# Kernel optimization log

Measured on AMD Instinct MI355X. Metric: run time of the kernel, lower is better.

The kernel has to match this reference:

```python
import jax, jax.numpy as jnp
import numpy as np

N = 50000      # num nodes
C_IN = 128     # channels[0]
C_OUT = 128    # channels[1]
D = 16         # fixed node degree
T = 4          # diffusion steps
H_MLP = 64     # diff_mlp hidden
H_GRU = 128    # GRUAggr hidden
EPS = 0.01


def setup_inputs() -> dict:
    key = jax.random.key(0)
    ks = jax.random.split(key, 10)
    node_attr = jax.random.normal(ks[0], (N, C_IN), jnp.float32)
    # adjacency sorted by source: node i owns columns [i*D, i*D+D)
    src = jnp.repeat(jnp.arange(N), D)
    dst = jax.random.randint(ks[1], (N * D,), 0, N)
    edge_index = jnp.stack([src, dst])                       # [2, N*D]
    slices = jnp.stack([jnp.arange(N) * D, jnp.full((N,), D)], axis=1)  # [N,2] (start,count)
    noise = EPS * jax.random.normal(ks[2], (T, N, D), jnp.float32)      # eps*randn per step
    init = lambda k, shape, fan: (jax.random.normal(k, shape, jnp.float32) / np.sqrt(fan))
    W1 = init(ks[3], ((1 + T) * C_IN, H_MLP), (1 + T) * C_IN)
    b1 = jnp.zeros((H_MLP,), jnp.float32)
    W2 = init(ks[4], (H_MLP, 1), H_MLP)
    b2 = jnp.zeros((1,), jnp.float32)
    Wx = init(ks[5], (C_IN, 3 * H_GRU), C_IN)
    Wh = init(ks[6], (H_GRU, 3 * H_GRU), H_GRU)
    bx = jnp.zeros((3 * H_GRU,), jnp.float32)
    bh = jnp.zeros((3 * H_GRU,), jnp.float32)
    Wo = init(ks[7], (H_GRU, C_OUT), H_GRU)
    bo = jnp.zeros((C_OUT,), jnp.float32)
    return dict(node_attr=node_attr, edge_index=edge_index, slices=slices, noise=noise,
                W1=W1, b1=b1, W2=W2, b2=b2, Wx=Wx, Wh=Wh, bx=bx, bh=bh, Wo=Wo, bo=bo)


def _gru(x_seq, Wx, Wh, bx, bh):
    # x_seq: [T+1, N, C]; torch GRU gate order (r, z, n)
    H = Wh.shape[0]
    def step(h, x):
        gx = x @ Wx + bx
        gh = h @ Wh + bh
        xr, xz, xn = jnp.split(gx, 3, axis=-1)
        hr, hz, hn = jnp.split(gh, 3, axis=-1)
        r = jax.nn.sigmoid(xr + hr)
        z = jax.nn.sigmoid(xz + hz)
        n = jnp.tanh(xn + r * hn)
        return (1.0 - z) * n + z * h, None
    h0 = jnp.zeros((x_seq.shape[1], H), x_seq.dtype)
    h, _ = jax.lax.scan(step, h0, x_seq)
    return h


def reference(node_attr, edge_index, slices, noise, W1, b1, W2, b2, Wx, Wh, bx, bh, Wo, bo):
    n, C = node_attr.shape
    t_steps, _, deg = noise.shape
    dst = edge_index[1]
    walk_embeds = jnp.zeros((n, 1 + t_steps, C), node_attr.dtype).at[:, 0, :].set(node_attr)
    cur = jnp.arange(n)
    for t in range(t_steps):
        starts = slices[cur, 0]                              # slice_cat(adj, adj_slic_t)
        nbr = dst[starts[:, None] + jnp.arange(deg)]         # [N, D] neighbor node ids
        v_t = node_attr[nbr]                                 # [N, D, C]
        # diff_mlp on [prefix walk embed | candidate neighbor]: split the first
        # linear layer so the shared prefix is computed once per node (position
        # 1+t of walk_embeds is still zero, matching the original fill order).
        h_pre = walk_embeds.reshape(n, (1 + t_steps) * C) @ W1 + b1       # [N, H_MLP]
        h_nbr = jnp.einsum('ndc,ch->ndh', v_t, W1[(1 + t) * C:(2 + t) * C])
        logp = (jax.nn.relu(h_pre[:, None, :] + h_nbr) @ W2)[..., 0] + b2[0]  # [N, D]
        logp = jax.lax.stop_gradient(logp)                   # torch.no_grad()
        # scatter_logsumexp over init node == logsumexp over the D candidates
        p = jnp.exp(logp - jax.nn.logsumexp(logp, axis=1, keepdims=True)) + noise[t]
        sel = jnp.argmax(p, axis=1)                          # scatter_max per init node
        cur = nbr[jnp.arange(n), sel]                        # walks_t
        walk_embeds = walk_embeds.at[:, 1 + t, :].set(node_attr[cur])
    h = _gru(jnp.transpose(walk_embeds, (1, 0, 2)), Wx, Wh, bx, bh)
    return h @ Wo + bo                                       # [N, C_OUT]
```

## Files before the change

### kernel.cpp

```cpp
#include <hip/hip_runtime.h>
#include <math.h>

#define NND 50000
#define DEG 16

typedef __attribute__((ext_vector_type(8))) short short8v;
typedef __attribute__((ext_vector_type(4))) float float4v;

#define OFF_HPRE 0ULL
#define OFF_PROJ 12800000ULL
#define OFF_XB   64000000ULL
#define OFF_IDX  102400000ULL
#define OFF_BQF  103600384ULL
#define OFF_WOF  103862528ULL
#define WS_NEED  103895296ULL

#define LOG2E 1.44269504088896f

__device__ __forceinline__ float fast_sig(float x){
    return __builtin_amdgcn_rcpf(1.f + __builtin_amdgcn_exp2f(-LOG2E*x));
}
__device__ __forceinline__ float fast_tanh(float x){
    return fmaf(-2.f, __builtin_amdgcn_rcpf(1.f + __builtin_amdgcn_exp2f((2.f*LOG2E)*x)), 1.f);
}
__device__ __forceinline__ unsigned short f2bf(float f){
    unsigned int u = __float_as_uint(f);
    u += 0x7FFFu + ((u >> 16) & 1u);
    return (unsigned short)(u >> 16);
}
__device__ __forceinline__ float bf2f(unsigned short h){
    return __uint_as_float(((unsigned int)h) << 16);
}

__global__ __launch_bounds__(256) void k_iota(int* __restrict__ idx0){
    int i = blockIdx.x*256 + threadIdx.x;
    if (i < NND) idx0[i] = i;
}

__global__ __launch_bounds__(256) void k_projall(const float* __restrict__ A,
    const float* __restrict__ W1, const float* __restrict__ b1,
    float* __restrict__ hpre, float* __restrict__ proj)
{
    __shared__ float Alt[32][320];
    __shared__ float Bl[32][68];
    const int tid = threadIdx.x;
    const int row0 = blockIdx.x << 8;
    const int y = blockIdx.y;
    const float* B = W1 + (size_t)y*128*64;
    const int row_t = tid >> 4, col_t = tid & 15;
    float4 acc[16];
#pragma unroll
    for (int i=0;i<16;i++) acc[i] = make_float4(0.f,0.f,0.f,0.f);

    for (int k0 = 0; k0 < 128; k0 += 32){
        {
            int gr = row0 + tid; if (gr >= NND) gr = NND-1;
            const float* ap = A + (size_t)gr*128 + k0;
            const int sr = tid + ((tid>>4)<<2);
#pragma unroll
            for (int u=0;u<8;u++){
                float4 v = *(const float4*)(ap + (u<<2));
                Alt[(u<<2)+0][sr] = v.x; Alt[(u<<2)+1][sr] = v.y;
                Alt[(u<<2)+2][sr] = v.z; Alt[(u<<2)+3][sr] = v.w;
            }
        }
#pragma unroll
        for (int r=0;r<2;r++){
            int p = (r<<8) + tid;
            int bk = p >> 4, bc = (p & 15) << 2;
            *(float4*)(&Bl[bk][bc]) = *(const float4*)(B + (size_t)(k0+bk)*64 + bc);
        }
        __syncthreads();
#pragma unroll 2
        for (int k=0;k<32;k++){
            const float* ar = &Alt[k][row_t*20];
            float4 a0 = *(const float4*)(ar);
            float4 a1 = *(const float4*)(ar+4);
            float4 a2 = *(const float4*)(ar+8);
            float4 a3 = *(const float4*)(ar+12);
            float4 b  = *(const float4*)(&Bl[k][col_t<<2]);
            float aa[16] = {a0.x,a0.y,a0.z,a0.w, a1.x,a1.y,a1.z,a1.w,
                            a2.x,a2.y,a2.z,a2.w, a3.x,a3.y,a3.z,a3.w};
#pragma unroll
            for (int j=0;j<16;j++){
                acc[j].x = fmaf(aa[j], b.x, acc[j].x);
                acc[j].y = fmaf(aa[j], b.y, acc[j].y);
                acc[j].z = fmaf(aa[j], b.z, acc[j].z);
                acc[j].w = fmaf(aa[j], b.w, acc[j].w);
            }
        }
        __syncthreads();
    }
    float4 bb = make_float4(0.f,0.f,0.f,0.f);
    if (y == 0) bb = *(const float4*)(b1 + (col_t<<2));
    float* dstp = (y == 0) ? hpre : (proj + (size_t)(y-1)*NND*64);
#pragma unroll
    for (int j=0;j<16;j++){
        int gr = row0 + (row_t<<4) + j;
        if (gr < NND){
            float4 o = make_float4(acc[j].x+bb.x, acc[j].y+bb.y, acc[j].z+bb.z, acc[j].w+bb.w);
            *(float4*)(dstp + ((size_t)gr<<6) + (col_t<<2)) = o;
        }
    }
}

__global__ __launch_bounds__(256) void k_walk4(
    const float* __restrict__ hpre0, const float* __restrict__ proj,
    const int* __restrict__ dst, const float* __restrict__ W2,
    const float* __restrict__ b2, const float* __restrict__ noise,
    int* __restrict__ idxb)
{
    const int tid = threadIdx.x;
    const int sg = tid >> 4, l = tid & 15;
    const int gi = (blockIdx.x << 4) + sg;
    float4 hp = *(const float4*)(hpre0 + ((size_t)gi<<6) + (l<<2));
    float4 w2 = *(const float4*)(W2 + (l<<2));
    const float b2s = b2[0];
    int curv = gi;
#pragma unroll 1
    for (int t=0; t<4; t++){
        const float* pj = proj + (size_t)t*NND*64;
        const int nbr = dst[curv*DEG + l];
        float4 val[16];
#pragma unroll
        for (int d=0; d<16; d++){
            int nd = __shfl(nbr, d, 16);
            val[d] = *(const float4*)(pj + ((size_t)nd<<6) + (l<<2));
        }
        float lp = 0.f;
#pragma unroll
        for (int d=0; d<16; d++){
            float4 v = val[d];
            float q =  fmaxf(hp.x+v.x,0.f)*w2.x;
            q = fmaf(fmaxf(hp.y+v.y,0.f), w2.y, q);
            q = fmaf(fmaxf(hp.z+v.z,0.f), w2.z, q);
            q = fmaf(fmaxf(hp.w+v.w,0.f), w2.w, q);
            q += __shfl_xor(q, 1, 16);
            q += __shfl_xor(q, 2, 16);
            q += __shfl_xor(q, 4, 16);
            q += __shfl_xor(q, 8, 16);
            if (l == d) lp = q + b2s;
        }
        float mx = lp;
#pragma unroll
        for (int off=8; off; off>>=1) mx = fmaxf(mx, __shfl_xor(mx, off, 16));
        float s = expf(lp - mx);
#pragma unroll
        for (int off=8; off; off>>=1) s += __shfl_xor(s, off, 16);
        float p = expf(lp - mx - logf(s)) + noise[(size_t)t*NND*DEG + ((size_t)gi<<4) + l];
        float bv = p; int bi = l;
#pragma unroll
        for (int off=8; off; off>>=1){
            float ov = __shfl_xor(bv, off, 16);
            int   oi = __shfl_xor(bi, off, 16);
            if (ov > bv || (ov == bv && oi < bi)){ bv = ov; bi = oi; }
        }
        int sel = __shfl(nbr, bi, 16);
        if (l == 0) idxb[(size_t)(t+1)*NND + gi] = sel;
        float4 u = *(const float4*)(pj + ((size_t)sel<<6) + (l<<2));
        hp.x += u.x; hp.y += u.y; hp.z += u.z; hp.w += u.w;
        curv = sel;
    }
}

__global__ __launch_bounds__(256) void k_pack_x(const float* __restrict__ na,
    unsigned short* __restrict__ Xb)
{
    int i = blockIdx.x*256 + threadIdx.x;
    if (i < NND*32){
        float4 v = *(const float4*)(na + (size_t)i*4);
        unsigned long long pk = (unsigned long long)f2bf(v.x)
            | ((unsigned long long)f2bf(v.y) << 16)
            | ((unsigned long long)f2bf(v.z) << 32)
            | ((unsigned long long)f2bf(v.w) << 48);
        *(unsigned long long*)(Xb + (size_t)i*4) = pk;
    }
}

__global__ __launch_bounds__(256) void k_pack_bqf(const float* __restrict__ Wx,
    const float* __restrict__ Wh, unsigned short* __restrict__ BqF)
{
    int i = blockIdx.x*256 + threadIdx.x;
    int jj = i & 7, lane = (i>>3)&63, ct = (i>>9)&7, c = (i>>12)&7, y = i>>15;
    int g = ct>>1, jh = ct&1, mm = lane&15, quad = lane>>4;
    int jg = (y<<5) + (jh<<4) + mm;
    int k = (c<<5) + (quad<<3) + jj;
    float v = 0.f;
    if (k < 128){
        if (g < 3) v = Wh[k*384 + g*128 + jg];
    } else {
        int kk = k - 128;
        if (g == 0)      v = Wx[kk*384 + jg];
        else if (g == 1) v = Wx[kk*384 + 128 + jg];
        else if (g == 3) v = Wx[kk*384 + 256 + jg];
    }
    BqF[i] = f2bf(v);
}

__global__ __launch_bounds__(256) void k_pack_wof(const float* __restrict__ Wo,
    unsigned short* __restrict__ WoF)
{
    int i = blockIdx.x*256 + threadIdx.x;
    int jj = i & 7, lane = (i>>3)&63, ct = (i>>9)&7, c = i>>12;
    int n = (ct<<4) + (lane&15);
    int k = (c<<5) + ((lane>>4)<<3) + jj;
    WoF[i] = f2bf(Wo[k*128 + n]);
}

__global__ __launch_bounds__(256,2) void k_gru5(
    const unsigned short* __restrict__ Xb,
    const unsigned short* __restrict__ BqF,
    const unsigned short* __restrict__ WoF,
    const float* __restrict__ bx, const float* __restrict__ bh,
    const float* __restrict__ bo, const int* __restrict__ idxb,
    float* __restrict__ out)
{
    __shared__ unsigned short A_l[8192];
    __shared__ unsigned short X_l[16384];
    const int tid = threadIdx.x;
    const int w = tid >> 6, lane = tid & 63;
    const int m = lane & 15, quad = lane >> 4;
    const int row0 = blockIdx.x << 6;
    const int r = tid & 63, q = tid >> 6;
    int gr = row0 + r; if (gr >= NND) gr = NND-1;
    const int rt_s = r >> 4, m_s = r & 15;
    float brr[2], bzz[2], bxn[2], bhn[2];
#pragma unroll
    for (int jh=0; jh<2; jh++){
        int j = (w<<5) + (jh<<4) + m;
        brr[jh] = bx[j] + bh[j];
        bzz[jh] = bx[128+j] + bh[128+j];
        bxn[jh] = bx[256+j];
        bhn[jh] = bh[256+j];
    }
    unsigned short holdv[2][4][4];
    short8v xv[4];
    {
        const int xr = idxb[gr];
        const unsigned short* xrow = Xb + (size_t)xr*128 + (q<<5);
#pragma unroll
        for (int u=0;u<4;u++) xv[u] = *(const short8v*)(xrow + (u<<3));
#pragma unroll
        for (int u=0;u<4;u++)
            *(short8v*)(X_l + (((rt_s<<2)+q)*64 + (u<<4) + m_s)*8) = xv[u];
        const int xr1 = idxb[NND + gr];
        const unsigned short* xrow1 = Xb + (size_t)xr1*128 + (q<<5);
#pragma unroll
        for (int u=0;u<4;u++) xv[u] = *(const short8v*)(xrow1 + (u<<3));
    }
    __syncthreads();

#pragma unroll 1
    for (int s=0; s<5; s++){
        const unsigned short* Xcur = X_l + ((s&1)<<13);
        float4v zero = {0.f,0.f,0.f,0.f};
        float4v acc[32];
#pragma unroll
        for (int i=0;i<32;i++) acc[i] = zero;
        if (s > 0){
#pragma unroll 1
            for (int c=0;c<4;c++){
                short8v afr[4];
#pragma unroll
                for (int rt=0;rt<4;rt++)
                    afr[rt] = *(const short8v*)(A_l + (((rt<<2) + c)*64 + lane)*8);
                const unsigned short* bp = BqF + ((((size_t)w*8 + c)*8)*64 + lane)*8;
#pragma unroll
                for (int ct=0;ct<6;ct++){
                    short8v bf = *(const short8v*)(bp + (ct<<9));
#pragma unroll
                    for (int rt=0;rt<4;rt++)
                        acc[(ct<<2)+rt] = __builtin_amdgcn_mfma_f32_16x16x32_bf16(afr[rt], bf, acc[(ct<<2)+rt], 0,0,0);
                }
            }
        }
#pragma unroll 1
        for (int c=4;c<8;c++){
            short8v afr[4];
#pragma unroll
            for (int rt=0;rt<4;rt++)
                afr[rt] = *(const short8v*)(Xcur + (((rt<<2) + (c&3))*64 + lane)*8);
            const unsigned short* bp = BqF + ((((size_t)w*8 + c)*8)*64 + lane)*8;
#pragma unroll
            for (int cti=0;cti<6;cti++){
                const int ct = (cti < 4) ? cti : (cti + 2);
                short8v bf = *(const short8v*)(bp + (ct<<9));
#pragma unroll
                for (int rt=0;rt<4;rt++)
                    acc[(ct<<2)+rt] = __builtin_amdgcn_mfma_f32_16x16x32_bf16(afr[rt], bf, acc[(ct<<2)+rt], 0,0,0);
            }
        }
        if (s < 4){
            unsigned short* Xnxt = X_l + (((s+1)&1)<<13);
#pragma unroll
            for (int u=0;u<4;u++)
                *(short8v*)(Xnxt + (((rt_s<<2)+q)*64 + (u<<4) + m_s)*8) = xv[u];
            if (s < 3){
                const int xr = idxb[(size_t)(s+2)*NND + gr];
                const unsigned short* xrow = Xb + (size_t)xr*128 + (q<<5);
#pragma unroll
                for (int u=0;u<4;u++) xv[u] = *(const short8v*)(xrow + (u<<3));
            }
        }
#pragma unroll
        for (int jh=0; jh<2; jh++){
#pragma unroll
            for (int rt=0; rt<4; rt++){
#pragma unroll
                for (int r4=0; r4<4; r4++){
                    float rg = fast_sig(acc[(jh<<2)+rt][r4] + brr[jh]);
                    float zg = fast_sig(acc[((2+jh)<<2)+rt][r4] + bzz[jh]);
                    float ng = fast_tanh(acc[((6+jh)<<2)+rt][r4] + bxn[jh] + rg*(acc[((4+jh)<<2)+rt][r4] + bhn[jh]));
                    float hold = (s == 0) ? 0.f : bf2f(holdv[jh][rt][r4]);
                    holdv[jh][rt][r4] = f2bf((1.f - zg)*ng + zg*hold);
                }
            }
        }
        __syncthreads();
#pragma unroll
        for (int jh=0; jh<2; jh++)
#pragma unroll
            for (int rt=0; rt<4; rt++)
#pragma unroll
                for (int r4=0; r4<4; r4++){
                    int ha = ((((rt<<2)+w)*64 + (((jh<<1)+(m>>3))<<4) + (quad<<2)+r4)<<3) + (m&7);
                    A_l[ha] = holdv[jh][rt][r4];
                }
        __syncthreads();
    }
    float4v zero = {0.f,0.f,0.f,0.f};
    float4v acco[8];
#pragma unroll
    for (int i=0;i<8;i++) acco[i] = zero;
    for (int c=0;c<4;c++){
        short8v afr[4];
#pragma unroll
        for (int rt=0;rt<4;rt++)
            afr[rt] = *(const short8v*)(A_l + (((rt<<2) + c)*64 + lane)*8);
#pragma unroll
        for (int cto=0;cto<2;cto++){
            short8v bf = *(const short8v*)(WoF + (((size_t)(c*8 + (w<<1)+cto))*64 + lane)*8);
#pragma unroll
            for (int rt=0;rt<4;rt++)
                acco[(cto<<2)+rt] = __builtin_amdgcn_mfma_f32_16x16x32_bf16(afr[rt], bf, acco[(cto<<2)+rt], 0,0,0);
        }
    }
#pragma unroll
    for (int cto=0; cto<2; cto++){
        int col = (w<<5) + (cto<<4) + m;
        float bb = bo[col];
#pragma unroll
        for (int rt=0; rt<4; rt++){
#pragma unroll
            for (int r4=0; r4<4; r4++){
                int row = row0 + (rt<<4) + (quad<<2) + r4;
                if (row < NND) out[(size_t)row*128 + col] = acco[(cto<<2)+rt][r4] + bb;
            }
        }
    }
}

extern "C" void kernel_launch(void* const* d_in, const int* in_sizes, int n_in,
                              void* d_out, int out_size, void* d_ws, size_t ws_size,
                              hipStream_t stream)
{
    const float* node_attr = (const float*)d_in[0];
    const int*   edge_index= (const int*)  d_in[1];
    const float* noise = (const float*)d_in[3];
    const float* W1 = (const float*)d_in[4];
    const float* b1 = (const float*)d_in[5];
    const float* W2 = (const float*)d_in[6];
    const float* b2 = (const float*)d_in[7];
    const float* Wx = (const float*)d_in[8];
    const float* Wh = (const float*)d_in[9];
    const float* bx = (const float*)d_in[10];
    const float* bh = (const float*)d_in[11];
    const float* Wo = (const float*)d_in[12];
    const float* bo = (const float*)d_in[13];
    const int* dst = edge_index + (size_t)NND*DEG;
    float* out = (float*)d_out;
    if (ws_size < WS_NEED) return;

    char* ws = (char*)d_ws;
    float* hpre = (float*)(ws + OFF_HPRE);
    float* proj = (float*)(ws + OFF_PROJ);
    unsigned short* Xb  = (unsigned short*)(ws + OFF_XB);
    int* idxb = (int*)(ws + OFF_IDX);
    unsigned short* BqF = (unsigned short*)(ws + OFF_BQF);
    unsigned short* WoF = (unsigned short*)(ws + OFF_WOF);

    k_iota<<<dim3(196), dim3(256), 0, stream>>>(idxb);
    k_pack_x  <<<dim3(6250), dim3(256), 0, stream>>>(node_attr, Xb);
    k_pack_bqf<<<dim3(512),  dim3(256), 0, stream>>>(Wx, Wh, BqF);
    k_pack_wof<<<dim3(64),   dim3(256), 0, stream>>>(Wo, WoF);

    k_projall<<<dim3(196, 5), dim3(256), 0, stream>>>(node_attr, W1, b1, hpre, proj);
    k_walk4<<<dim3(3125), dim3(256), 0, stream>>>(hpre, proj, dst, W2, b2, noise, idxb);

    k_gru5<<<dim3(782), dim3(256), 0, stream>>>(Xb, BqF, WoF, bx, bh, bo, idxb, out);
}
```

Measured before the change: 358.4 us.

## Fuse setup kernels, persist GRU blocks, double-buffer hidden state in LDS

Four small preprocessing kernels (bf16 packing of node features, GRU and output weights, plus index init) are merged into one launch. The GRU kernel becomes a grid-stride loop over 512 blocks covering 782 row tiles, sized to two blocks per CU. The hidden-state LDS buffer is double-buffered, so the barrier before writing the new state is no longer needed. This cuts launch overhead and one barrier per step, at the cost of doubling the hidden-state LDS buffer (64 KB per block) and some load imbalance, since some blocks process two tiles and others one.

```diff
diff --git a/kernel.cpp b/kernel.cpp
--- a/kernel.cpp
+++ b/kernel.cpp
@@ -32,9 +32,50 @@
     return __uint_as_float(((unsigned int)h) << 16);
 }
 
-__global__ __launch_bounds__(256) void k_iota(int* __restrict__ idx0){
-    int i = blockIdx.x*256 + threadIdx.x;
-    if (i < NND) idx0[i] = i;
+__global__ __launch_bounds__(256) void k_setup(const float* __restrict__ na,
+    const float* __restrict__ Wx, const float* __restrict__ Wh,
+    const float* __restrict__ Wo, unsigned short* __restrict__ Xb,
+    unsigned short* __restrict__ BqF, unsigned short* __restrict__ WoF,
+    int* __restrict__ idx0)
+{
+    const int b = blockIdx.x, tid = threadIdx.x;
+    {
+        int i = b*256 + tid;
+        if (i < NND*32){
+            float4 v = *(const float4*)(na + (size_t)i*4);
+            unsigned long long pk = (unsigned long long)f2bf(v.x)
+                | ((unsigned long long)f2bf(v.y) << 16)
+                | ((unsigned long long)f2bf(v.z) << 32)
+                | ((unsigned long long)f2bf(v.w) << 48);
+            *(unsigned long long*)(Xb + (size_t)i*4) = pk;
+        }
+    }
+    if (b < 512){
+        int i = b*256 + tid;
+        int jj = i & 7, lane = (i>>3)&63, ct = (i>>9)&7, c = (i>>12)&7, y = i>>15;
+        int g = ct>>1, jh = ct&1, mm = lane&15, quad = lane>>4;
+        int jg = (y<<5) + (jh<<4) + mm;
+        int k = (c<<5) + (quad<<3) + jj;
+        float v = 0.f;
+        if (k < 128){
+            if (g < 3) v = Wh[k*384 + g*128 + jg];
+        } else {
+            int kk = k - 128;
+            if (g == 0)      v = Wx[kk*384 + jg];
+            else if (g == 1) v = Wx[kk*384 + 128 + jg];
+            else if (g == 3) v = Wx[kk*384 + 256 + jg];
+        }
+        BqF[i] = f2bf(v);
+    } else if (b < 576){
+        int i = (b-512)*256 + tid;
+        int jj = i & 7, lane = (i>>3)&63, ct = (i>>9)&7, c = i>>12;
+        int n = (ct<<4) + (lane&15);
+        int k = (c<<5) + ((lane>>4)<<3) + jj;
+        WoF[i] = f2bf(Wo[k*128 + n]);
+    } else if (b < 772){
+        int i = (b-576)*256 + tid;
+        if (i < NND) idx0[i] = i;
+    }
 }
 
 __global__ __launch_bounds__(256) void k_projall(const float* __restrict__ A,
@@ -163,50 +204,6 @@
     }
 }
 
-__global__ __launch_bounds__(256) void k_pack_x(const float* __restrict__ na,
-    unsigned short* __restrict__ Xb)
-{
-    int i = blockIdx.x*256 + threadIdx.x;
-    if (i < NND*32){
-        float4 v = *(const float4*)(na + (size_t)i*4);
-        unsigned long long pk = (unsigned long long)f2bf(v.x)
-            | ((unsigned long long)f2bf(v.y) << 16)
-            | ((unsigned long long)f2bf(v.z) << 32)
-            | ((unsigned long long)f2bf(v.w) << 48);
-        *(unsigned long long*)(Xb + (size_t)i*4) = pk;
-    }
-}
-
-__global__ __launch_bounds__(256) void k_pack_bqf(const float* __restrict__ Wx,
-    const float* __restrict__ Wh, unsigned short* __restrict__ BqF)
-{
-    int i = blockIdx.x*256 + threadIdx.x;
-    int jj = i & 7, lane = (i>>3)&63, ct = (i>>9)&7, c = (i>>12)&7, y = i>>15;
-    int g = ct>>1, jh = ct&1, mm = lane&15, quad = lane>>4;
-    int jg = (y<<5) + (jh<<4) + mm;
-    int k = (c<<5) + (quad<<3) + jj;
-    float v = 0.f;
-    if (k < 128){
-        if (g < 3) v = Wh[k*384 + g*128 + jg];
-    } else {
-        int kk = k - 128;
-        if (g == 0)      v = Wx[kk*384 + jg];
-        else if (g == 1) v = Wx[kk*384 + 128 + jg];
-        else if (g == 3) v = Wx[kk*384 + 256 + jg];
-    }
-    BqF[i] = f2bf(v);
-}
-
-__global__ __launch_bounds__(256) void k_pack_wof(const float* __restrict__ Wo,
-    unsigned short* __restrict__ WoF)
-{
-    int i = blockIdx.x*256 + threadIdx.x;
-    int jj = i & 7, lane = (i>>3)&63, ct = (i>>9)&7, c = i>>12;
-    int n = (ct<<4) + (lane&15);
-    int k = (c<<5) + ((lane>>4)<<3) + jj;
-    WoF[i] = f2bf(Wo[k*128 + n]);
-}
-
 __global__ __launch_bounds__(256,2) void k_gru5(
     const unsigned short* __restrict__ Xb,
     const unsigned short* __restrict__ BqF,
@@ -215,14 +212,12 @@
     const float* __restrict__ bo, const int* __restrict__ idxb,
     float* __restrict__ out)
 {
-    __shared__ unsigned short A_l[8192];
+    __shared__ unsigned short A_l[2][8192];
     __shared__ unsigned short X_l[16384];
     const int tid = threadIdx.x;
     const int w = tid >> 6, lane = tid & 63;
     const int m = lane & 15, quad = lane >> 4;
-    const int row0 = blockIdx.x << 6;
     const int r = tid & 63, q = tid >> 6;
-    int gr = row0 + r; if (gr >= NND) gr = NND-1;
     const int rt_s = r >> 4, m_s = r & 15;
     float brr[2], bzz[2], bxn[2], bhn[2];
 #pragma unroll
@@ -233,128 +228,137 @@
         bxn[jh] = bx[256+j];
         bhn[jh] = bh[256+j];
     }
-    unsigned short holdv[2][4][4];
-    short8v xv[4];
-    {
-        const int xr = idxb[gr];
-        const unsigned short* xrow = Xb + (size_t)xr*128 + (q<<5);
-#pragma unroll
-        for (int u=0;u<4;u++) xv[u] = *(const short8v*)(xrow + (u<<3));
-#pragma unroll
-        for (int u=0;u<4;u++)
-            *(short8v*)(X_l + (((rt_s<<2)+q)*64 + (u<<4) + m_s)*8) = xv[u];
-        const int xr1 = idxb[NND + gr];
-        const unsigned short* xrow1 = Xb + (size_t)xr1*128 + (q<<5);
-#pragma unroll
-        for (int u=0;u<4;u++) xv[u] = *(const short8v*)(xrow1 + (u<<3));
-    }
-    __syncthreads();
-
-#pragma unroll 1
-    for (int s=0; s<5; s++){
-        const unsigned short* Xcur = X_l + ((s&1)<<13);
-        float4v zero = {0.f,0.f,0.f,0.f};
-        float4v acc[32];
-#pragma unroll
-        for (int i=0;i<32;i++) acc[i] = zero;
-        if (s > 0){
-#pragma unroll 1
-            for (int c=0;c<4;c++){
+
+#pragma unroll 1
+    for (int tb = blockIdx.x; tb < 782; tb += 512){
+        const int row0 = tb << 6;
+        int gr = row0 + r; if (gr >= NND) gr = NND-1;
+        unsigned short holdv[2][4][4];
+        short8v xv[4];
+        {
+            const int xr = idxb[gr];
+            const unsigned short* xrow = Xb + (size_t)xr*128 + (q<<5);
+#pragma unroll
+            for (int u=0;u<4;u++) xv[u] = *(const short8v*)(xrow + (u<<3));
+#pragma unroll
+            for (int u=0;u<4;u++)
+                *(short8v*)(X_l + (((rt_s<<2)+q)*64 + (u<<4) + m_s)*8) = xv[u];
+            const int xr1 = idxb[NND + gr];
+            const unsigned short* xrow1 = Xb + (size_t)xr1*128 + (q<<5);
+#pragma unroll
+            for (int u=0;u<4;u++) xv[u] = *(const short8v*)(xrow1 + (u<<3));
+        }
+        __syncthreads();
+
+#pragma unroll 1
+        for (int s=0; s<5; s++){
+            const unsigned short* Acur = A_l[s&1];
+            const unsigned short* Xcur = X_l + ((s&1)<<13);
+            float4v zero = {0.f,0.f,0.f,0.f};
+            float4v acc[32];
+#pragma unroll
+            for (int i=0;i<32;i++) acc[i] = zero;
+            if (s > 0){
+#pragma unroll 1
+                for (int c=0;c<4;c++){
+                    short8v afr[4];
+#pragma unroll
+                    for (int rt=0;rt<4;rt++)
+                        afr[rt] = *(const short8v*)(Acur + (((rt<<2) + c)*64 + lane)*8);
+                    const unsigned short* bp = BqF + ((((size_t)w*8 + c)*8)*64 + lane)*8;
+#pragma unroll
+                    for (int ct=0;ct<6;ct++){
+                        short8v bf = *(const short8v*)(bp + (ct<<9));
+#pragma unroll
+                        for (int rt=0;rt<4;rt++)
+                            acc[(ct<<2)+rt] = __builtin_amdgcn_mfma_f32_16x16x32_bf16(afr[rt], bf, acc[(ct<<2)+rt], 0,0,0);
+                    }
+                }
+            }
+#pragma unroll 1
+            for (int c=4;c<8;c++){
                 short8v afr[4];
 #pragma unroll
                 for (int rt=0;rt<4;rt++)
-                    afr[rt] = *(const short8v*)(A_l + (((rt<<2) + c)*64 + lane)*8);
+                    afr[rt] = *(const short8v*)(Xcur + (((rt<<2) + (c&3))*64 + lane)*8);
                 const unsigned short* bp = BqF + ((((size_t)w*8 + c)*8)*64 + lane)*8;
 #pragma unroll
-                for (int ct=0;ct<6;ct++){
+                for (int cti=0;cti<6;cti++){
+                    const int ct = (cti < 4) ? cti : (cti + 2);
                     short8v bf = *(const short8v*)(bp + (ct<<9));
 #pragma unroll
                     for (int rt=0;rt<4;rt++)
                         acc[(ct<<2)+rt] = __builtin_amdgcn_mfma_f32_16x16x32_bf16(afr[rt], bf, acc[(ct<<2)+rt], 0,0,0);
                 }
             }
-        }
-#pragma unroll 1
-        for (int c=4;c<8;c++){
+            if (s < 4){
+                unsigned short* Xnxt = X_l + (((s+1)&1)<<13);
+#pragma unroll
+                for (int u=0;u<4;u++)
+                    *(short8v*)(Xnxt + (((rt_s<<2)+q)*64 + (u<<4) + m_s)*8) = xv[u];
+                if (s < 3){
+                    const int xr = idxb[(size_t)(s+2)*NND + gr];
+                    const unsigned short* xrow = Xb + (size_t)xr*128 + (q<<5);
+#pragma unroll
+                    for (int u=0;u<4;u++) xv[u] = *(const short8v*)(xrow + (u<<3));
+                }
+            }
+#pragma unroll
+            for (int jh=0; jh<2; jh++){
+#pragma unroll
+                for (int rt=0; rt<4; rt++){
+#pragma unroll
+                    for (int r4=0; r4<4; r4++){
+                        float rg = fast_sig(acc[(jh<<2)+rt][r4] + brr[jh]);
+                        float zg = fast_sig(acc[((2+jh)<<2)+rt][r4] + bzz[jh]);
+                        float ng = fast_tanh(acc[((6+jh)<<2)+rt][r4] + bxn[jh] + rg*(acc[((4+jh)<<2)+rt][r4] + bhn[jh]));
+                        float hold = (s == 0) ? 0.f : bf2f(holdv[jh][rt][r4]);
+                        holdv[jh][rt][r4] = f2bf((1.f - zg)*ng + zg*hold);
+                    }
+                }
+            }
+            unsigned short* Anxt = A_l[(s+1)&1];
+#pragma unroll
+            for (int jh=0; jh<2; jh++)
+#pragma unroll
+                for (int rt=0; rt<4; rt++)
+#pragma unroll
+                    for (int r4=0; r4<4; r4++){
+                        int ha = ((((rt<<2)+w)*64 + (((jh<<1)+(m>>3))<<4) + (quad<<2)+r4)<<3) + (m&7);
+                        Anxt[ha] = holdv[jh][rt][r4];
+                    }
+            __syncthreads();
+        }
+        const unsigned short* Afin = A_l[1];
+        float4v zero = {0.f,0.f,0.f,0.f};
+        float4v acco[8];
+#pragma unroll
+        for (int i=0;i<8;i++) acco[i] = zero;
+#pragma unroll 1
+        for (int c=0;c<4;c++){
             short8v afr[4];
 #pragma unroll
             for (int rt=0;rt<4;rt++)
-                afr[rt] = *(const short8v*)(Xcur + (((rt<<2) + (c&3))*64 + lane)*8);
-            const unsigned short* bp = BqF + ((((size_t)w*8 + c)*8)*64 + lane)*8;
-#pragma unroll
-            for (int cti=0;cti<6;cti++){
-                const int ct = (cti < 4) ? cti : (cti + 2);
-                short8v bf = *(const short8v*)(bp + (ct<<9));
+                afr[rt] = *(const short8v*)(Afin + (((rt<<2) + c)*64 + lane)*8);
+#pragma unroll
+            for (int cto=0;cto<2;cto++){
+                short8v bf = *(const short8v*)(WoF + (((size_t)(c*8 + (w<<1)+cto))*64 + lane)*8);
 #pragma unroll
                 for (int rt=0;rt<4;rt++)
-                    acc[(ct<<2)+rt] = __builtin_amdgcn_mfma_f32_16x16x32_bf16(afr[rt], bf, acc[(ct<<2)+rt], 0,0,0);
-            }
-        }
-        if (s < 4){
-            unsigned short* Xnxt = X_l + (((s+1)&1)<<13);
-#pragma unroll
-            for (int u=0;u<4;u++)
-                *(short8v*)(Xnxt + (((rt_s<<2)+q)*64 + (u<<4) + m_s)*8) = xv[u];
-            if (s < 3){
-                const int xr = idxb[(size_t)(s+2)*NND + gr];
-                const unsigned short* xrow = Xb + (size_t)xr*128 + (q<<5);
-#pragma unroll
-                for (int u=0;u<4;u++) xv[u] = *(const short8v*)(xrow + (u<<3));
-            }
-        }
-#pragma unroll
-        for (int jh=0; jh<2; jh++){
+                    acco[(cto<<2)+rt] = __builtin_amdgcn_mfma_f32_16x16x32_bf16(afr[rt], bf, acco[(cto<<2)+rt], 0,0,0);
+            }
+        }
+#pragma unroll
+        for (int cto=0; cto<2; cto++){
+            int col = (w<<5) + (cto<<4) + m;
+            float bb = bo[col];
 #pragma unroll
             for (int rt=0; rt<4; rt++){
 #pragma unroll
                 for (int r4=0; r4<4; r4++){
-                    float rg = fast_sig(acc[(jh<<2)+rt][r4] + brr[jh]);
-                    float zg = fast_sig(acc[((2+jh)<<2)+rt][r4] + bzz[jh]);
-                    float ng = fast_tanh(acc[((6+jh)<<2)+rt][r4] + bxn[jh] + rg*(acc[((4+jh)<<2)+rt][r4] + bhn[jh]));
-                    float hold = (s == 0) ? 0.f : bf2f(holdv[jh][rt][r4]);
-                    holdv[jh][rt][r4] = f2bf((1.f - zg)*ng + zg*hold);
+                    int row = row0 + (rt<<4) + (quad<<2) + r4;
+                    if (row < NND) out[(size_t)row*128 + col] = acco[(cto<<2)+rt][r4] + bb;
                 }
-            }
-        }
-        __syncthreads();
-#pragma unroll
-        for (int jh=0; jh<2; jh++)
-#pragma unroll
-            for (int rt=0; rt<4; rt++)
-#pragma unroll
-                for (int r4=0; r4<4; r4++){
-                    int ha = ((((rt<<2)+w)*64 + (((jh<<1)+(m>>3))<<4) + (quad<<2)+r4)<<3) + (m&7);
-                    A_l[ha] = holdv[jh][rt][r4];
-                }
-        __syncthreads();
-    }
-    float4v zero = {0.f,0.f,0.f,0.f};
-    float4v acco[8];
-#pragma unroll
-    for (int i=0;i<8;i++) acco[i] = zero;
-    for (int c=0;c<4;c++){
-        short8v afr[4];
-#pragma unroll
-        for (int rt=0;rt<4;rt++)
-            afr[rt] = *(const short8v*)(A_l + (((rt<<2) + c)*64 + lane)*8);
-#pragma unroll
-        for (int cto=0;cto<2;cto++){
-            short8v bf = *(const short8v*)(WoF + (((size_t)(c*8 + (w<<1)+cto))*64 + lane)*8);
-#pragma unroll
-            for (int rt=0;rt<4;rt++)
-                acco[(cto<<2)+rt] = __builtin_amdgcn_mfma_f32_16x16x32_bf16(afr[rt], bf, acco[(cto<<2)+rt], 0,0,0);
-        }
-    }
-#pragma unroll
-    for (int cto=0; cto<2; cto++){
-        int col = (w<<5) + (cto<<4) + m;
-        float bb = bo[col];
-#pragma unroll
-        for (int rt=0; rt<4; rt++){
-#pragma unroll
-            for (int r4=0; r4<4; r4++){
-                int row = row0 + (rt<<4) + (quad<<2) + r4;
-                if (row < NND) out[(size_t)row*128 + col] = acco[(cto<<2)+rt][r4] + bb;
             }
         }
     }
@@ -389,13 +393,10 @@
     unsigned short* BqF = (unsigned short*)(ws + OFF_BQF);
     unsigned short* WoF = (unsigned short*)(ws + OFF_WOF);
 
-    k_iota<<<dim3(196), dim3(256), 0, stream>>>(idxb);
-    k_pack_x  <<<dim3(6250), dim3(256), 0, stream>>>(node_attr, Xb);
-    k_pack_bqf<<<dim3(512),  dim3(256), 0, stream>>>(Wx, Wh, BqF);
-    k_pack_wof<<<dim3(64),   dim3(256), 0, stream>>>(Wo, WoF);
+    k_setup<<<dim3(6250), dim3(256), 0, stream>>>(node_attr, Wx, Wh, Wo, Xb, BqF, WoF, idxb);
 
     k_projall<<<dim3(196, 5), dim3(256), 0, stream>>>(node_attr, W1, b1, hpre, proj);
     k_walk4<<<dim3(3125), dim3(256), 0, stream>>>(hpre, proj, dst, W2, b2, noise, idxb);
 
-    k_gru5<<<dim3(782), dim3(256), 0, stream>>>(Xb, BqF, WoF, bx, bh, bo, idxb, out);
-}
+    k_gru5<<<dim3(512), dim3(256), 0, stream>>>(Xb, BqF, WoF, bx, bh, bo, idxb, out);
+}
```

Measured after the change: 358.1 us. About the same (-0.1%).
